# Kernel tuning notes

Hardware: AMD Instinct MI355X
Metric: run time of the kernel (lower is better)

Reference implementation:

```python
import jax, jax.numpy as jnp
import numpy as np
from jax import lax

B, T, E, H, L, V = 64, 512, 512, 1024, 2, 32000  # batch, seq, d_emb, d_hid, n_layer, n_vocab


def setup_inputs() -> dict:
    key = jax.random.key(0)
    ks = jax.random.split(key, 8)
    s = 0.03  # small init keeps tanh recurrence well-conditioned
    return {
        "src": jax.random.randint(ks[0], (B, T), 0, V),
        "emb_table": jax.random.normal(ks[1], (V, E), jnp.float32) * s,
        "W1": jax.random.normal(ks[2], (H, E), jnp.float32) * s,
        "b1": jnp.zeros((H,), jnp.float32),
        "W2": jax.random.normal(ks[3], (H, H), jnp.float32) * s,
        "b2": jnp.zeros((H,), jnp.float32),
        # layer 0 input dim = H; layers >0 input dim = 2H (bidirectional concat)
        "W_ih0": jax.random.normal(ks[4], (2, H, H), jnp.float32) * s,
        "W_ihL": jax.random.normal(ks[5], (L - 1, 2, H, 2 * H), jnp.float32) * s,
        "W_hh": jax.random.normal(ks[6], (L, 2, H, H), jnp.float32) * s,
        "b_ih": jnp.zeros((L, 2, H), jnp.float32),
        "b_hh": jnp.zeros((L, 2, H), jnp.float32),
    }


def _rnn_dir(x, Wih, Whh, bih, bhh, reverse):
    # x: [B, T, Din]. Precompute input projection as one big GEMM, then scan.
    pre = jnp.einsum('bti,hi->tbh', x, Wih) + bih  # [T, B, H]

    def step(h, p):
        h = jnp.tanh(p + h @ Whh.T + bhh)
        return h, h

    h0 = jnp.zeros((x.shape[0], Whh.shape[0]), x.dtype)
    hT, hs = lax.scan(step, h0, pre, reverse=reverse)
    return hT, jnp.transpose(hs, (1, 0, 2))  # final state [B,H], outputs [B,T,H]


def reference(src, emb_table, W1, b1, W2, b2, W_ih0, W_ihL, W_hh, b_ih, b_hh):
    # Embedding with padding_idx=0 (row zeroed)
    table = emb_table.at[0].set(0.0)
    x = table[src]  # [B, T, E]
    # emb_to_hid MLP (dropout is identity in eval mode)
    x = jax.nn.relu(x @ W1.T + b1)
    x = jax.nn.relu(x @ W2.T + b2)  # [B, T, H]
    finals = []
    inp = x
    for l in range(L):
        Wih = W_ih0 if l == 0 else W_ihL[l - 1]
        hf, of = _rnn_dir(inp, Wih[0], W_hh[l, 0], b_ih[l, 0], b_hh[l, 0], False)
        hb, ob = _rnn_dir(inp, Wih[1], W_hh[l, 1], b_ih[l, 1], b_hh[l, 1], True)
        finals += [hf, hb]
        inp = jnp.concatenate([of, ob], axis=-1)  # [B, T, 2H]
    # torch h_n layout: [n_layer * num_directions, B, H], layer-major, dir-minor
    return jnp.stack(finals, axis=0)
```

## Files before the change

### kernel.cpp

```cpp
#include <hip/hip_runtime.h>


typedef _Float16 f16;
typedef _Float16 f16x8 __attribute__((ext_vector_type(8)));
typedef _Float16 f16x4 __attribute__((ext_vector_type(4)));
typedef float f32x4 __attribute__((ext_vector_type(4)));

static const size_t MB_ = 1024ull * 1024ull;
static const size_t OFF_X0    = 0;
static const size_t OFF_X1    = 64 * MB_;
static const size_t OFF_EMB   = OFF_X1;
static const size_t OFF_MLP1  = 96 * MB_;
static const size_t OFF_H     = 192 * MB_;
static const size_t OFF_FLAGS = 192 * MB_ + 512 * 1024;
static const size_t OFF_BIAS  = 192 * MB_ + 576 * 1024;
static const size_t OFF_W1C   = 193 * MB_;
static const size_t OFF_W2C   = 194 * MB_;
static const size_t WS_NEED   = 196 * MB_;
static const size_t P_PRE1D0 = 0;
static const size_t P_PRE1D1 = 192 * MB_;
static const size_t P_HB1    = 64 * MB_;
static const size_t P_FL1    = 64 * MB_ + 512 * 1024;
static const size_t P_BIAS1  = 64 * MB_ + 528 * 1024;
static const size_t WS_NEED2 = 256 * MB_;

__device__ __forceinline__ void gld16(const void* g, void* l) {
#if __has_builtin(__builtin_amdgcn_global_load_lds)
  __builtin_amdgcn_global_load_lds((const __attribute__((address_space(1))) void*)g,
                                   (__attribute__((address_space(3))) void*)l, 16, 0, 0);
#else
  *(f16x8*)l = *(const f16x8*)g;
#endif
}

__device__ __forceinline__ float tanh_fast(float x) {
  float ax = __builtin_fabsf(x);
  float e = __builtin_amdgcn_exp2f(ax * 2.8853900817779268f);
  float r = 1.0f - 2.0f * __builtin_amdgcn_rcpf(e + 1.0f);
  return __builtin_copysignf(r, x);
}


__global__ void zero_k(unsigned int* __restrict__ p, int n) {
  int i = blockIdx.x * blockDim.x + threadIdx.x;
  if (i < n) p[i] = 0u;
}

__global__ void cvt_k(const float* __restrict__ in, f16* __restrict__ out, int n4) {
  int i = blockIdx.x * blockDim.x + threadIdx.x;
  int stride = gridDim.x * blockDim.x;
  for (; i < n4; i += stride) {
    float4 v = ((const float4*)in)[i];
    f16x4 o = {(f16)v.x, (f16)v.y, (f16)v.z, (f16)v.w};
    ((f16x4*)out)[i] = o;
  }
}

__global__ void bias_k(const float* __restrict__ a, const float* __restrict__ b, float* __restrict__ o) {
  int i = blockIdx.x * blockDim.x + threadIdx.x;
  if (i < 4096) o[i] = a[i] + b[i];
}

__global__ void embed_k(const int* __restrict__ src, const float* __restrict__ tab, f16* __restrict__ out) {
  int m = blockIdx.x;
  int tid = threadIdx.x;
  int tok = src[m];
  f16x4 o = {(f16)0.f, (f16)0.f, (f16)0.f, (f16)0.f};
  if (tok != 0) {
    float4 v = *(const float4*)(tab + (size_t)tok * 512 + tid * 4);
    o[0] = (f16)v.x; o[1] = (f16)v.y; o[2] = (f16)v.z; o[3] = (f16)v.w;
  }
  *(f16x4*)(out + (size_t)m * 512 + tid * 4) = o;
}

template <int EPI>
__global__ __launch_bounds__(256) void gemm_f16(
    const f16* __restrict__ A, int lda, const f16* __restrict__ Bw,
    f16* __restrict__ out, const float* __restrict__ bias, int M, int N, int K) {
  __shared__ alignas(16) f16 As[4096];
  __shared__ alignas(16) f16 Bs[4096];
  const int nt = N >> 7;
  const int bx = blockIdx.x;
  const int tm = bx / nt, tn = bx - tm * nt;
  const int tid = threadIdx.x;
  const int l = tid & 63, w = tid >> 6;
  const int wr = w >> 1, wc = w & 1;
  const int srow = (w << 4) + (l >> 2);
  const int scol = (l & 3) << 3;
  const f16* Ab = A + (size_t)(tm * 128 + srow) * lda + scol;
  const f16* Bb = Bw + (size_t)(tn * 128 + srow) * K + scol;
  f32x4 acc[4][4];
#pragma unroll
  for (int i = 0; i < 4; i++)
#pragma unroll
    for (int j = 0; j < 4; j++) acc[i][j] = (f32x4){0.f, 0.f, 0.f, 0.f};
  const int ar = l & 15, ak = (l >> 4) << 3;
  for (int k0 = 0; k0 < K; k0 += 32) {
    gld16(Ab + k0, &As[tid * 8]);
    gld16(Ab + (size_t)64 * lda + k0, &As[tid * 8 + 2048]);
    gld16(Bb + k0, &Bs[tid * 8]);
    gld16(Bb + (size_t)64 * K + k0, &Bs[tid * 8 + 2048]);
    __syncthreads();
    f16x8 av[4], bv[4];
#pragma unroll
    for (int i = 0; i < 4; i++) av[i] = *(const f16x8*)&As[(wr * 64 + i * 16 + ar) * 32 + ak];
#pragma unroll
    for (int j = 0; j < 4; j++) bv[j] = *(const f16x8*)&Bs[(wc * 64 + j * 16 + ar) * 32 + ak];
#pragma unroll
    for (int i = 0; i < 4; i++)
#pragma unroll
      for (int j = 0; j < 4; j++)
        acc[i][j] = __builtin_amdgcn_mfma_f32_16x16x32_f16(av[i], bv[j], acc[i][j], 0, 0, 0);
    __syncthreads();
  }
  const int r0 = (l >> 4) << 2, c0 = l & 15;
#pragma unroll
  for (int i = 0; i < 4; i++) {
#pragma unroll
    for (int j = 0; j < 4; j++) {
      const int col = tn * 128 + wc * 64 + j * 16 + c0;
      const float bc = (EPI & 1) ? bias[col] : 0.f;
#pragma unroll
      for (int r = 0; r < 4; r++) {
        const int row = tm * 128 + wr * 64 + i * 16 + r0 + r;
        float v = acc[i][j][r];
        if (EPI & 1) { v += bc; v = v > 0.f ? v : 0.f; }
        if (EPI & 2) {
          const int b_ = row >> 9, t = row & 511;
          out[((size_t)(t * 64 + b_) << 10) + col] = (f16)v;
        } else {
          out[(size_t)row * N + col] = (f16)v;
        }
      }
    }
  }
}

__global__ __launch_bounds__(256) void gemm_b32(
    const f16* __restrict__ A, int lda, const float* __restrict__ Bw,
    f16* __restrict__ out, int M, int N, int K) {
  __shared__ alignas(16) f16 As[4096];
  __shared__ alignas(16) f16 Bs[4096];
  const int nt = N >> 7;
  const int bx = blockIdx.x;
  const int tm = bx / nt, tn = bx - tm * nt;
  const int tid = threadIdx.x;
  const int l = tid & 63, w = tid >> 6;
  const int wr = w >> 1, wc = w & 1;
  const int srow = (w << 4) + (l >> 2);
  const int scol = (l & 3) << 3;
  const f16* Ab = A + (size_t)(tm * 128 + srow) * lda + scol;
  const int brow = tid >> 1, bcol = (tid & 1) << 4;
  const float* Bb = Bw + (size_t)(tn * 128 + brow) * K + bcol;
  f32x4 acc[4][4];
#pragma unroll
  for (int i = 0; i < 4; i++)
#pragma unroll
    for (int j = 0; j < 4; j++) acc[i][j] = (f32x4){0.f, 0.f, 0.f, 0.f};
  const int ar = l & 15, ak = (l >> 4) << 3;
  for (int k0 = 0; k0 < K; k0 += 32) {
    gld16(Ab + k0, &As[tid * 8]);
    gld16(Ab + (size_t)64 * lda + k0, &As[tid * 8 + 2048]);
    {
      const float* bp = Bb + k0;
      float4 u0 = *(const float4*)(bp + 0), u1 = *(const float4*)(bp + 4);
      float4 u2 = *(const float4*)(bp + 8), u3 = *(const float4*)(bp + 12);
      f16x8 h0 = {(f16)u0.x, (f16)u0.y, (f16)u0.z, (f16)u0.w,
                  (f16)u1.x, (f16)u1.y, (f16)u1.z, (f16)u1.w};
      f16x8 h1 = {(f16)u2.x, (f16)u2.y, (f16)u2.z, (f16)u2.w,
                  (f16)u3.x, (f16)u3.y, (f16)u3.z, (f16)u3.w};
      *(f16x8*)&Bs[brow * 32 + bcol] = h0;
      *(f16x8*)&Bs[brow * 32 + bcol + 8] = h1;
    }
    __syncthreads();
    f16x8 av[4], bv[4];
#pragma unroll
    for (int i = 0; i < 4; i++) av[i] = *(const f16x8*)&As[(wr * 64 + i * 16 + ar) * 32 + ak];
#pragma unroll
    for (int j = 0; j < 4; j++) bv[j] = *(const f16x8*)&Bs[(wc * 64 + j * 16 + ar) * 32 + ak];
#pragma unroll
    for (int i = 0; i < 4; i++)
#pragma unroll
      for (int j = 0; j < 4; j++)
        acc[i][j] = __builtin_amdgcn_mfma_f32_16x16x32_f16(av[i], bv[j], acc[i][j], 0, 0, 0);
    __syncthreads();
  }
  const int r0 = (l >> 4) << 2, c0 = l & 15;
#pragma unroll
  for (int i = 0; i < 4; i++) {
#pragma unroll
    for (int j = 0; j < 4; j++) {
      const int col = tn * 128 + wc * 64 + j * 16 + c0;
#pragma unroll
      for (int r = 0; r < 4; r++) {
        const int row = tm * 128 + wr * 64 + i * 16 + r0 + r;
        out[(size_t)row * N + col] = (f16)acc[i][j][r];
      }
    }
  }
}

template <int LAYER>
__global__ __launch_bounds__(512, 1) void rnn_scan(
    const f16* __restrict__ X, const float* __restrict__ Wih, const float* __restrict__ Whh,
    const float* __restrict__ bsum, f16* __restrict__ hbuf, unsigned int* __restrict__ flags,
    f16* __restrict__ seqout, float* __restrict__ dout) {
  constexpr int KX = LAYER ? 2048 : 1024;
  constexpr int XSH = LAYER ? 11 : 10;
  constexpr int NKX = KX / 128;
  constexpr int NKH = 8;
  const int bid = blockIdx.x;
  const int g_ = (bid & 7) >> 1;
  const int dir = g_ >> 1, bg = g_ & 1;
  const int cg = ((bid & 1) << 5) | (bid >> 3);
  const int tid = threadIdx.x, l = tid & 63, w = tid >> 6;
  const int mi = w & 1, kq = w >> 1;
  __shared__ alignas(16) f16 Wl[16 * 1024];
  __shared__ alignas(16) f16 Wi[16 * KX];
  __shared__ f32x4 part[2][4][64];
  __shared__ alignas(16) f16 p2[32][16];
  __shared__ unsigned int cnt;
  const int ld = LAYER * 2 + dir;
  if (tid == 0) cnt = 0u;
  for (int ch = tid; ch < 2048; ch += 512) {
    const int n = ch >> 7, k0 = (ch & 127) << 3;
    const float* wp = Whh + (((size_t)(ld * 1024 + cg * 16 + n)) << 10) + k0;
    float4 v0 = *(const float4*)wp, v1 = *(const float4*)(wp + 4);
    f16x8 hv = {(f16)v0.x, (f16)v0.y, (f16)v0.z, (f16)v0.w,
                (f16)v1.x, (f16)v1.y, (f16)v1.z, (f16)v1.w};
    *(f16x8*)&Wl[(n << 10) + (k0 ^ ((n & 7) << 3))] = hv;
  }
  for (int ch = tid; ch < (16 * KX / 8); ch += 512) {
    const int n = ch >> (XSH - 3), k0 = (ch & (KX / 8 - 1)) << 3;
    const float* wp = Wih + ((size_t)(dir * 1024 + cg * 16 + n)) * KX + k0;
    float4 v0 = *(const float4*)wp, v1 = *(const float4*)(wp + 4);
    f16x8 hv = {(f16)v0.x, (f16)v0.y, (f16)v0.z, (f16)v0.w,
                (f16)v1.x, (f16)v1.y, (f16)v1.z, (f16)v1.w};
    *(f16x8*)&Wi[(n << XSH) + (k0 ^ ((n & 7) << 3))] = hv;
  }
  const float bn = bsum[(ld << 10) + cg * 16 + (l & 15)];
  f16* hD = hbuf + ((size_t)dir << 17);
  unsigned int* fl = flags + ((dir * 2 + bg) << 10);
  const int arow = bg * 32 + mi * 16 + (l & 15);
  const int akh = (kq << 8) + ((l >> 4) << 3);
  const int akx = kq * (KX / 4) + ((l >> 4) << 3);
  const int wn = l & 15;
  const int wsw = (wn & 7) << 3;

  f16x8 xv[NKX];
  {
    const int t0 = dir ? 511 : 0;
    const f16* xr = X + (((size_t)(t0 * 64 + arow)) << XSH) + akx;
#pragma unroll
    for (int i = 0; i < NKX; i++)
      asm volatile("global_load_dwordx4 %0, %1, off offset:%2"
                   : "=&v"(xv[i]) : "v"(xr), "i"(64 * i));
  }
  __syncthreads();

  for (int s = 0; s < 512; ++s) {
    const int t = dir ? (511 - s) : s;
    f32x4 acc = {0.f, 0.f, 0.f, 0.f};
    if (s > 0) {
      if (w == 7) {
        const unsigned int tgt = (unsigned int)(LAYER * 512 + s);
        unsigned int* fp = fl + l * 16;
        for (;;) {
          unsigned int f = __hip_atomic_load(fp, __ATOMIC_RELAXED, __HIP_MEMORY_SCOPE_AGENT);
          if (__all((int)(f >= tgt))) break;
        }
      }
      __syncthreads();
      const f16* hrow = hD + (((size_t)(s & 1)) << 16) + (((size_t)arow) << 10) + akh;
      f16x8 hv[NKH];
#pragma unroll
      for (int i = 0; i < NKH; i++)
        asm volatile("global_load_dwordx4 %0, %1, off offset:%2 sc0 sc1"
                     : "=&v"(hv[i]) : "v"(hrow), "i"(64 * i));
      asm volatile("s_waitcnt vmcnt(%0)" :: "i"(NKH) : "memory");
      __builtin_amdgcn_sched_barrier(0);
#pragma unroll
      for (int it = 0; it < NKX; ++it) {
        const int ko = akx + it * 32;
        f16x8 bv = *(const f16x8*)&Wi[(wn << XSH) + (ko ^ wsw)];
        acc = __builtin_amdgcn_mfma_f32_16x16x32_f16(xv[it], bv, acc, 0, 0, 0);
      }
      asm volatile("s_waitcnt vmcnt(0)" ::: "memory");
      __builtin_amdgcn_sched_barrier(0);
#pragma unroll
      for (int it = 0; it < NKH; ++it) {
        const int ko = akh + it * 32;
        f16x8 bv = *(const f16x8*)&Wl[(wn << 10) + (ko ^ wsw)];
        acc = __builtin_amdgcn_mfma_f32_16x16x32_f16(hv[it], bv, acc, 0, 0, 0);
      }
    } else {
      asm volatile("s_waitcnt vmcnt(0)" ::: "memory");
      __builtin_amdgcn_sched_barrier(0);
#pragma unroll
      for (int it = 0; it < NKX; ++it) {
        const int ko = akx + it * 32;
        f16x8 bv = *(const f16x8*)&Wi[(wn << XSH) + (ko ^ wsw)];
        acc = __builtin_amdgcn_mfma_f32_16x16x32_f16(xv[it], bv, acc, 0, 0, 0);
      }
    }
    part[mi][kq][l] = acc;
    __syncthreads();
    if (w < 2) {
      f32x4 sum = part[w][0][l];
      sum += part[w][1][l];
      sum += part[w][2][l];
      sum += part[w][3][l];
#pragma unroll
      for (int r = 0; r < 4; ++r) {
        const int row = ((l >> 4) << 2) + r;
        float v = tanh_fast(sum[r] + bn);
        p2[(w << 4) + row][l & 15] = (f16)v;
        if (s == 511) {
          const int b_ = bg * 32 + (w << 4) + row;
          dout[(((size_t)(ld * 64 + b_)) << 10) + cg * 16 + (l & 15)] = v;
        }
      }
      asm volatile("s_waitcnt lgkmcnt(0)" ::: "memory");
      __builtin_amdgcn_sched_barrier(0);
      if (l < 32) {
        const int rr = (w << 4) + (l >> 1), hf = l & 1;
        f16x8 pv = *(const f16x8*)&p2[rr][hf * 8];
        const int b_ = bg * 32 + rr;
        f16* hp = hD + (((size_t)((s + 1) & 1)) << 16) + (((size_t)b_) << 10) + cg * 16 + hf * 8;
        asm volatile("global_store_dwordx4 %0, %1, off sc0 sc1" :: "v"(hp), "v"(pv) : "memory");
        if (LAYER == 0) {
          f16* sp = seqout + (((size_t)(t * 64 + b_)) << 11) + (dir << 10) + cg * 16 + hf * 8;
          asm volatile("global_store_dwordx4 %0, %1, off" :: "v"(sp), "v"(pv) : "memory");
        }
      }
      asm volatile("s_waitcnt vmcnt(0)" ::: "memory");
      __builtin_amdgcn_sched_barrier(0);
      if (l == 0) {
        unsigned int old = __hip_atomic_fetch_add(&cnt, 1u, __ATOMIC_RELAXED,
                                                  __HIP_MEMORY_SCOPE_WORKGROUP);
        if (old == (unsigned int)(2 * s + 1))
          __hip_atomic_store(&fl[cg * 16], (unsigned int)(LAYER * 512 + s + 1),
                             __ATOMIC_RELAXED, __HIP_MEMORY_SCOPE_AGENT);
      }
    }
    if (s + 1 < 512) {
      const int tn_ = dir ? (511 - (s + 1)) : (s + 1);
      const f16* xr = X + (((size_t)(tn_ * 64 + arow)) << XSH) + akx;
#pragma unroll
      for (int i = 0; i < NKX; i++)
        asm volatile("global_load_dwordx4 %0, %1, off offset:%2"
                     : "=&v"(xv[i]) : "v"(xr), "i"(64 * i));
    }
  }
}

__global__ __launch_bounds__(512, 1) void rnn_scan_pre1(
    const f16* __restrict__ PRE0,
    const f16* __restrict__ PRE1,
    const float* __restrict__ Whh,
    const float* __restrict__ bsum,
    f16* __restrict__ hbuf,
    unsigned int* __restrict__ flags,
    float* __restrict__ dout) {
  constexpr int NKH = 8;
  const int bid = blockIdx.x;
  const int g_ = (bid & 7) >> 1;
  const int dir = g_ >> 1, bg = g_ & 1;
  const int cg = ((bid & 1) << 5) | (bid >> 3);
  const int tid = threadIdx.x, l = tid & 63, w = tid >> 6;
  const int mi = w & 1, kq = w >> 1;
  __shared__ alignas(16) f16 Wl[16 * 1024];
  __shared__ f32x4 part[2][4][64];
  __shared__ alignas(16) f16 p2[32][16];
  __shared__ unsigned int cnt;
  const int ld = 2 + dir;
  if (tid == 0) cnt = 0u;
  for (int ch = tid; ch < 2048; ch += 512) {
    const int n = ch >> 7, k0 = (ch & 127) << 3;
    const float* wp = Whh + (((size_t)(ld * 1024 + cg * 16 + n)) << 10) + k0;
    float4 v0 = *(const float4*)wp, v1 = *(const float4*)(wp + 4);
    f16x8 hv = {(f16)v0.x, (f16)v0.y, (f16)v0.z, (f16)v0.w,
                (f16)v1.x, (f16)v1.y, (f16)v1.z, (f16)v1.w};
    *(f16x8*)&Wl[(n << 10) + (k0 ^ ((n & 7) << 3))] = hv;
  }
  const int pcol = cg * 16 + (l & 15);
  const float bn = bsum[(ld << 10) + pcol];
  const f16* preD = dir ? PRE1 : PRE0;
  f16* hD = hbuf + ((size_t)dir << 17);
  unsigned int* fl = flags + ((dir * 2 + bg) << 10);
  const int arow = bg * 32 + mi * 16 + (l & 15);
  const int akh = (kq << 8) + ((l >> 4) << 3);
  const int wn = l & 15;
  const int wsw = (wn & 7) << 3;
  const int prow = bg * 32 + (w << 4) + ((l >> 4) << 2);

  unsigned int pu0 = 0, pu1 = 0, pu2 = 0, pu3 = 0;
  if (w < 2) {
    const int t0 = dir ? 511 : 0;
    const f16* ppA = preD + (((size_t)(t0 * 64 + prow)) << 10) + pcol;
    const f16* ppB = ppA + 2048;
    asm volatile("global_load_ushort %0, %1, off" : "=&v"(pu0) : "v"(ppA));
    asm volatile("global_load_ushort %0, %1, off offset:2048" : "=&v"(pu1) : "v"(ppA));
    asm volatile("global_load_ushort %0, %1, off" : "=&v"(pu2) : "v"(ppB));
    asm volatile("global_load_ushort %0, %1, off offset:2048" : "=&v"(pu3) : "v"(ppB));
  }
  __syncthreads();

  for (int s = 0; s < 512; ++s) {
    f32x4 acc = {0.f, 0.f, 0.f, 0.f};
    if (s > 0) {
      if (w == 7) {
        const unsigned int tgt = (unsigned int)s;
        unsigned int* fp = fl + l * 16;
        for (;;) {
          unsigned int f = __hip_atomic_load(fp, __ATOMIC_RELAXED, __HIP_MEMORY_SCOPE_AGENT);
          if (__all((int)(f >= tgt))) break;
        }
      }
      __syncthreads();
      const f16* hrow = hD + (((size_t)(s & 1)) << 16) + (((size_t)arow) << 10) + akh;
      f16x8 hv[NKH];
#pragma unroll
      for (int i = 0; i < NKH; i++)
        asm volatile("global_load_dwordx4 %0, %1, off offset:%2 sc0 sc1"
                     : "=&v"(hv[i]) : "v"(hrow), "i"(64 * i));
      asm volatile("s_waitcnt vmcnt(0)" ::: "memory");
      __builtin_amdgcn_sched_barrier(0);
#pragma unroll
      for (int it = 0; it < NKH; ++it) {
        const int ko = akh + it * 32;
        f16x8 bv = *(const f16x8*)&Wl[(wn << 10) + (ko ^ wsw)];
        acc = __builtin_amdgcn_mfma_f32_16x16x32_f16(hv[it], bv, acc, 0, 0, 0);
      }
    }
    part[mi][kq][l] = acc;
    __syncthreads();
    if (w < 2) {
      asm volatile("s_waitcnt vmcnt(0)" ::: "memory");
      __builtin_amdgcn_sched_barrier(0);
      float pva[4];
      pva[0] = (float)__builtin_bit_cast(f16, (unsigned short)pu0);
      pva[1] = (float)__builtin_bit_cast(f16, (unsigned short)pu1);
      pva[2] = (float)__builtin_bit_cast(f16, (unsigned short)pu2);
      pva[3] = (float)__builtin_bit_cast(f16, (unsigned short)pu3);
      f32x4 sum = part[w][0][l];
      sum += part[w][1][l];
      sum += part[w][2][l];
      sum += part[w][3][l];
#pragma unroll
      for (int r = 0; r < 4; ++r) {
        const int row = ((l >> 4) << 2) + r;
        float v = tanh_fast(sum[r] + pva[r] + bn);
        p2[(w << 4) + row][l & 15] = (f16)v;
        if (s == 511) {
          const int b_ = bg * 32 + (w << 4) + row;
          dout[(((size_t)(ld * 64 + b_)) << 10) + pcol] = v;
        }
      }
      asm volatile("s_waitcnt lgkmcnt(0)" ::: "memory");
      __builtin_amdgcn_sched_barrier(0);
      if (l < 32) {
        const int rr = (w << 4) + (l >> 1), hf = l & 1;
        f16x8 pv = *(const f16x8*)&p2[rr][hf * 8];
        const int b_ = bg * 32 + rr;
        f16* hp = hD + (((size_t)((s + 1) & 1)) << 16) + (((size_t)b_) << 10) + cg * 16 + hf * 8;
        asm volatile("global_store_dwordx4 %0, %1, off sc0 sc1" :: "v"(hp), "v"(pv) : "memory");
      }
      asm volatile("s_waitcnt vmcnt(0)" ::: "memory");
      __builtin_amdgcn_sched_barrier(0);
      if (l == 0) {
        unsigned int old = __hip_atomic_fetch_add(&cnt, 1u, __ATOMIC_RELAXED,
                                                  __HIP_MEMORY_SCOPE_WORKGROUP);
        if (old == (unsigned int)(2 * s + 1))
          __hip_atomic_store(&fl[cg * 16], (unsigned int)(s + 1),
                             __ATOMIC_RELAXED, __HIP_MEMORY_SCOPE_AGENT);
      }
      if (s + 1 < 512) {
        const int tn_ = dir ? (511 - (s + 1)) : (s + 1);
        const f16* ppA = preD + (((size_t)(tn_ * 64 + prow)) << 10) + pcol;
        const f16* ppB = ppA + 2048;
        asm volatile("global_load_ushort %0, %1, off" : "=&v"(pu0) : "v"(ppA));
        asm volatile("global_load_ushort %0, %1, off offset:2048" : "=&v"(pu1) : "v"(ppA));
        asm volatile("global_load_ushort %0, %1, off" : "=&v"(pu2) : "v"(ppB));
        asm volatile("global_load_ushort %0, %1, off offset:2048" : "=&v"(pu3) : "v"(ppB));
      }
    }
  }
}


extern "C" void kernel_launch(void* const* d_in, const int* in_sizes, int n_in,
                              void* d_out, int out_size, void* d_ws, size_t ws_size,
                              hipStream_t stream) {
  const int* src    = (const int*)d_in[0];
  const float* emb  = (const float*)d_in[1];
  const float* W1   = (const float*)d_in[2];
  const float* b1   = (const float*)d_in[3];
  const float* W2   = (const float*)d_in[4];
  const float* b2   = (const float*)d_in[5];
  const float* Wih0 = (const float*)d_in[6];
  const float* WihL = (const float*)d_in[7];
  const float* Whh  = (const float*)d_in[8];
  const float* bih  = (const float*)d_in[9];
  const float* bhh  = (const float*)d_in[10];
  float* out = (float*)d_out;
  char* ws = (char*)d_ws;

  if (ws_size < WS_NEED) {
    zero_k<<<(out_size + 255) / 256, 256, 0, stream>>>((unsigned int*)d_out, out_size);
    return;
  }

  f16* X0   = (f16*)(ws + OFF_X0);
  f16* X1   = (f16*)(ws + OFF_X1);
  f16* EMB  = (f16*)(ws + OFF_EMB);
  f16* MLP1 = (f16*)(ws + OFF_MLP1);
  f16* HB   = (f16*)(ws + OFF_H);
  unsigned int* FLAGS = (unsigned int*)(ws + OFF_FLAGS);
  float* BIAS = (float*)(ws + OFF_BIAS);
  f16* W1C  = (f16*)(ws + OFF_W1C);
  f16* W2C  = (f16*)(ws + OFF_W2C);

  cvt_k<<<256, 256, 0, stream>>>(W1, W1C, 131072);
  cvt_k<<<256, 256, 0, stream>>>(W2, W2C, 262144);
  bias_k<<<16, 256, 0, stream>>>(bih, bhh, BIAS);
  zero_k<<<16, 256, 0, stream>>>(FLAGS, 4096);

  embed_k<<<32768, 128, 0, stream>>>(src, emb, EMB);
  gemm_f16<1><<<2048, 256, 0, stream>>>(EMB, 512, W1C, MLP1, b1, 32768, 1024, 512);
  gemm_f16<3><<<2048, 256, 0, stream>>>(MLP1, 1024, W2C, X0, b2, 32768, 1024, 1024);

  rnn_scan<0><<<256, 512, 0, stream>>>(X0, Wih0, Whh, BIAS, HB, FLAGS, X1, out);

  if (ws_size >= WS_NEED2) {
    f16* PRE1D0 = (f16*)(ws + P_PRE1D0);
    f16* PRE1D1 = (f16*)(ws + P_PRE1D1);
    f16* HB1    = (f16*)(ws + P_HB1);
    unsigned int* FLAGS1 = (unsigned int*)(ws + P_FL1);
    float* BIAS1 = (float*)(ws + P_BIAS1);

    gemm_b32<<<2048, 256, 0, stream>>>(X1, 2048, WihL, PRE1D0, 32768, 1024, 2048);
    gemm_b32<<<2048, 256, 0, stream>>>(X1, 2048, WihL + (1u << 21), PRE1D1, 32768, 1024, 2048);

    zero_k<<<16, 256, 0, stream>>>(FLAGS1, 4096);
    bias_k<<<16, 256, 0, stream>>>(bih, bhh, BIAS1);

    rnn_scan_pre1<<<256, 512, 0, stream>>>(PRE1D0, PRE1D1, Whh, BIAS1, HB1, FLAGS1, out);
    return;
  }

  rnn_scan<1><<<256, 512, 0, stream>>>(X1, WihL, Whh, BIAS, HB, FLAGS, nullptr, out);
}
```

Baseline: 5.126 ms.

## Precompute layer-0 input projection with GEMM and reuse buffers in-place for outputs

Layer 0 no longer fuses the input projection into the sequential scan. Its input projection is now precomputed by two large GEMMs, the same way layer 1 already works. The layer-0 scan reuses the generic precomputed-input scan and writes each step's hidden state back into its own pre-activation buffer in place. A new GEMM variant then reads the two direction buffers as a virtual concatenated K=2048 input for layer 1. The goal is to move the per-step input-projection work off the latency-bound recurrence, at the cost of extra GEMM launches and memory traffic.

```diff
diff --git a/kernel.cpp b/kernel.cpp
--- a/kernel.cpp
+++ b/kernel.cpp
@@ -17,11 +17,21 @@
 static const size_t OFF_W1C   = 193 * MB_;
 static const size_t OFF_W2C   = 194 * MB_;
 static const size_t WS_NEED   = 196 * MB_;
-static const size_t P_PRE1D0 = 0;
-static const size_t P_PRE1D1 = 192 * MB_;
-static const size_t P_HB1    = 64 * MB_;
-static const size_t P_FL1    = 64 * MB_ + 512 * 1024;
-static const size_t P_BIAS1  = 64 * MB_ + 528 * 1024;
+static const size_t Q_X0     = 0;
+static const size_t Q_EMB    = 64 * MB_;
+static const size_t Q_MLP1   = 96 * MB_;
+static const size_t Q_W1C    = 160 * MB_;
+static const size_t Q_W2C    = 161 * MB_;
+static const size_t Q_PRE0D0 = 64 * MB_;
+static const size_t Q_PRE0D1 = 128 * MB_;
+static const size_t Q_HB0    = 192 * MB_;
+static const size_t Q_FL0    = 192 * MB_ + 512 * 1024;
+static const size_t Q_BIAS0  = 192 * MB_ + 544 * 1024;
+static const size_t Q_PRE1D0 = 0;
+static const size_t Q_PRE1D1 = 192 * MB_;
+static const size_t Q_HB1    = 64 * MB_;
+static const size_t Q_FL1    = 64 * MB_ + 512 * 1024;
+static const size_t Q_BIAS1  = 64 * MB_ + 544 * 1024;
 static const size_t WS_NEED2 = 256 * MB_;
 
 __device__ __forceinline__ void gld16(const void* g, void* l) {
@@ -161,6 +171,73 @@
   for (int k0 = 0; k0 < K; k0 += 32) {
     gld16(Ab + k0, &As[tid * 8]);
     gld16(Ab + (size_t)64 * lda + k0, &As[tid * 8 + 2048]);
+    {
+      const float* bp = Bb + k0;
+      float4 u0 = *(const float4*)(bp + 0), u1 = *(const float4*)(bp + 4);
+      float4 u2 = *(const float4*)(bp + 8), u3 = *(const float4*)(bp + 12);
+      f16x8 h0 = {(f16)u0.x, (f16)u0.y, (f16)u0.z, (f16)u0.w,
+                  (f16)u1.x, (f16)u1.y, (f16)u1.z, (f16)u1.w};
+      f16x8 h1 = {(f16)u2.x, (f16)u2.y, (f16)u2.z, (f16)u2.w,
+                  (f16)u3.x, (f16)u3.y, (f16)u3.z, (f16)u3.w};
+      *(f16x8*)&Bs[brow * 32 + bcol] = h0;
+      *(f16x8*)&Bs[brow * 32 + bcol + 8] = h1;
+    }
+    __syncthreads();
+    f16x8 av[4], bv[4];
+#pragma unroll
+    for (int i = 0; i < 4; i++) av[i] = *(const f16x8*)&As[(wr * 64 + i * 16 + ar) * 32 + ak];
+#pragma unroll
+    for (int j = 0; j < 4; j++) bv[j] = *(const f16x8*)&Bs[(wc * 64 + j * 16 + ar) * 32 + ak];
+#pragma unroll
+    for (int i = 0; i < 4; i++)
+#pragma unroll
+      for (int j = 0; j < 4; j++)
+        acc[i][j] = __builtin_amdgcn_mfma_f32_16x16x32_f16(av[i], bv[j], acc[i][j], 0, 0, 0);
+    __syncthreads();
+  }
+  const int r0 = (l >> 4) << 2, c0 = l & 15;
+#pragma unroll
+  for (int i = 0; i < 4; i++) {
+#pragma unroll
+    for (int j = 0; j < 4; j++) {
+      const int col = tn * 128 + wc * 64 + j * 16 + c0;
+#pragma unroll
+      for (int r = 0; r < 4; r++) {
+        const int row = tm * 128 + wr * 64 + i * 16 + r0 + r;
+        out[(size_t)row * N + col] = (f16)acc[i][j][r];
+      }
+    }
+  }
+}
+
+__global__ __launch_bounds__(256) void gemm_b32c(
+    const f16* __restrict__ A0, const f16* __restrict__ A1, const float* __restrict__ Bw,
+    f16* __restrict__ out, int M, int N) {
+  constexpr int K = 2048;
+  __shared__ alignas(16) f16 As[4096];
+  __shared__ alignas(16) f16 Bs[4096];
+  const int nt = N >> 7;
+  const int bx = blockIdx.x;
+  const int tm = bx / nt, tn = bx - tm * nt;
+  const int tid = threadIdx.x;
+  const int l = tid & 63, w = tid >> 6;
+  const int wr = w >> 1, wc = w & 1;
+  const int srow = (w << 4) + (l >> 2);
+  const int scol = (l & 3) << 3;
+  const int brow = tid >> 1, bcol = (tid & 1) << 4;
+  const float* Bb = Bw + (size_t)(tn * 128 + brow) * K + bcol;
+  f32x4 acc[4][4];
+#pragma unroll
+  for (int i = 0; i < 4; i++)
+#pragma unroll
+    for (int j = 0; j < 4; j++) acc[i][j] = (f32x4){0.f, 0.f, 0.f, 0.f};
+  const int ar = l & 15, ak = (l >> 4) << 3;
+  for (int k0 = 0; k0 < K; k0 += 32) {
+    const f16* base = (k0 < 1024) ? A0 : A1;
+    const int ko = k0 & 1023;
+    const f16* Ab = base + (size_t)(tm * 128 + srow) * 1024 + ko + scol;
+    gld16(Ab, &As[tid * 8]);
+    gld16(Ab + (size_t)64 * 1024, &As[tid * 8 + 2048]);
     {
       const float* bp = Bb + k0;
       float4 u0 = *(const float4*)(bp + 0), u1 = *(const float4*)(bp + 4);
@@ -354,9 +431,10 @@
   }
 }
 
-__global__ __launch_bounds__(512, 1) void rnn_scan_pre1(
-    const f16* __restrict__ PRE0,
-    const f16* __restrict__ PRE1,
+template <int LAYER>
+__global__ __launch_bounds__(512, 1) void rnn_scan_pre(
+    f16* __restrict__ PRE0,
+    f16* __restrict__ PRE1,
     const float* __restrict__ Whh,
     const float* __restrict__ bsum,
     f16* __restrict__ hbuf,
@@ -373,7 +451,7 @@
   __shared__ f32x4 part[2][4][64];
   __shared__ alignas(16) f16 p2[32][16];
   __shared__ unsigned int cnt;
-  const int ld = 2 + dir;
+  const int ld = LAYER * 2 + dir;
   if (tid == 0) cnt = 0u;
   for (int ch = tid; ch < 2048; ch += 512) {
     const int n = ch >> 7, k0 = (ch & 127) << 3;
@@ -385,7 +463,7 @@
   }
   const int pcol = cg * 16 + (l & 15);
   const float bn = bsum[(ld << 10) + pcol];
-  const f16* preD = dir ? PRE1 : PRE0;
+  f16* preD = dir ? PRE1 : PRE0;
   f16* hD = hbuf + ((size_t)dir << 17);
   unsigned int* fl = flags + ((dir * 2 + bg) << 10);
   const int arow = bg * 32 + mi * 16 + (l & 15);
@@ -407,6 +485,7 @@
   __syncthreads();
 
   for (int s = 0; s < 512; ++s) {
+    const int t = dir ? (511 - s) : s;
     f32x4 acc = {0.f, 0.f, 0.f, 0.f};
     if (s > 0) {
       if (w == 7) {
@@ -465,6 +544,10 @@
         const int b_ = bg * 32 + rr;
         f16* hp = hD + (((size_t)((s + 1) & 1)) << 16) + (((size_t)b_) << 10) + cg * 16 + hf * 8;
         asm volatile("global_store_dwordx4 %0, %1, off sc0 sc1" :: "v"(hp), "v"(pv) : "memory");
+        if (LAYER == 0) {
+          f16* xp = preD + (((size_t)(t * 64 + b_)) << 10) + cg * 16 + hf * 8;
+          asm volatile("global_store_dwordx4 %0, %1, off" :: "v"(xp), "v"(pv) : "memory");
+        }
       }
       asm volatile("s_waitcnt vmcnt(0)" ::: "memory");
       __builtin_amdgcn_sched_barrier(0);
@@ -511,6 +594,44 @@
     return;
   }
 
+  if (ws_size >= WS_NEED2) {
+    f16* X0    = (f16*)(ws + Q_X0);
+    f16* EMB   = (f16*)(ws + Q_EMB);
+    f16* MLP1  = (f16*)(ws + Q_MLP1);
+    f16* W1C   = (f16*)(ws + Q_W1C);
+    f16* W2C   = (f16*)(ws + Q_W2C);
+    f16* PRE0D0 = (f16*)(ws + Q_PRE0D0);
+    f16* PRE0D1 = (f16*)(ws + Q_PRE0D1);
+    f16* HB0   = (f16*)(ws + Q_HB0);
+    unsigned int* FL0 = (unsigned int*)(ws + Q_FL0);
+    float* BIAS0 = (float*)(ws + Q_BIAS0);
+    f16* PRE1D0 = (f16*)(ws + Q_PRE1D0);
+    f16* PRE1D1 = (f16*)(ws + Q_PRE1D1);
+    f16* HB1   = (f16*)(ws + Q_HB1);
+    unsigned int* FL1 = (unsigned int*)(ws + Q_FL1);
+    float* BIAS1 = (float*)(ws + Q_BIAS1);
+
+    cvt_k<<<256, 256, 0, stream>>>(W1, W1C, 131072);
+    cvt_k<<<256, 256, 0, stream>>>(W2, W2C, 262144);
+
+    embed_k<<<32768, 128, 0, stream>>>(src, emb, EMB);
+    gemm_f16<1><<<2048, 256, 0, stream>>>(EMB, 512, W1C, MLP1, b1, 32768, 1024, 512);
+    gemm_f16<3><<<2048, 256, 0, stream>>>(MLP1, 1024, W2C, X0, b2, 32768, 1024, 1024);
+
+    gemm_b32<<<2048, 256, 0, stream>>>(X0, 1024, Wih0, PRE0D0, 32768, 1024, 1024);
+    gemm_b32<<<2048, 256, 0, stream>>>(X0, 1024, Wih0 + (1u << 20), PRE0D1, 32768, 1024, 1024);
+    zero_k<<<16, 256, 0, stream>>>(FL0, 4096);
+    bias_k<<<16, 256, 0, stream>>>(bih, bhh, BIAS0);
+    rnn_scan_pre<0><<<256, 512, 0, stream>>>(PRE0D0, PRE0D1, Whh, BIAS0, HB0, FL0, out);
+
+    gemm_b32c<<<2048, 256, 0, stream>>>(PRE0D0, PRE0D1, WihL, PRE1D0, 32768, 1024);
+    gemm_b32c<<<2048, 256, 0, stream>>>(PRE0D0, PRE0D1, WihL + (1u << 21), PRE1D1, 32768, 1024);
+    zero_k<<<16, 256, 0, stream>>>(FL1, 4096);
+    bias_k<<<16, 256, 0, stream>>>(bih, bhh, BIAS1);
+    rnn_scan_pre<1><<<256, 512, 0, stream>>>(PRE1D0, PRE1D1, Whh, BIAS1, HB1, FL1, out);
+    return;
+  }
+
   f16* X0   = (f16*)(ws + OFF_X0);
   f16* X1   = (f16*)(ws + OFF_X1);
   f16* EMB  = (f16*)(ws + OFF_EMB);
@@ -531,23 +652,5 @@
   gemm_f16<3><<<2048, 256, 0, stream>>>(MLP1, 1024, W2C, X0, b2, 32768, 1024, 1024);
 
   rnn_scan<0><<<256, 512, 0, stream>>>(X0, Wih0, Whh, BIAS, HB, FLAGS, X1, out);
-
-  if (ws_size >= WS_NEED2) {
-    f16* PRE1D0 = (f16*)(ws + P_PRE1D0);
-    f16* PRE1D1 = (f16*)(ws + P_PRE1D1);
-    f16* HB1    = (f16*)(ws + P_HB1);
-    unsigned int* FLAGS1 = (unsigned int*)(ws + P_FL1);
-    float* BIAS1 = (float*)(ws + P_BIAS1);
-
-    gemm_b32<<<2048, 256, 0, stream>>>(X1, 2048, WihL, PRE1D0, 32768, 1024, 2048);
-    gemm_b32<<<2048, 256, 0, stream>>>(X1, 2048, WihL + (1u << 21), PRE1D1, 32768, 1024, 2048);
-
-    zero_k<<<16, 256, 0, stream>>>(FLAGS1, 4096);
-    bias_k<<<16, 256, 0, stream>>>(bih, bhh, BIAS1);
-
-    rnn_scan_pre1<<<256, 512, 0, stream>>>(PRE1D0, PRE1D1, Whh, BIAS1, HB1, FLAGS1, out);
-    return;
-  }
-
   rnn_scan<1><<<256, 512, 0, stream>>>(X1, WihL, Whh, BIAS, HB, FLAGS, nullptr, out);
 }
```

Result: faster. 5.000 ms (-2.5%).
